# Kernel tuning notes

Measured on AMD Instinct MI355X. Metric: run time of the kernel, lower is better.

## Reference

```python
import jax, jax.numpy as jnp
import numpy as np

N_NODES = 20000
N_EDGES = 640000
IN_DIM, HID_DIM, OUT_DIM = 128, 128, 64


def setup_inputs() -> dict:
    key = jax.random.key(0)
    k = jax.random.split(key, 6)
    x = jax.random.normal(k[0], (N_NODES, IN_DIM), dtype=jnp.float32)
    edge_index = jax.random.randint(k[1], (2, N_EDGES), 0, N_NODES, dtype=jnp.int64)
    W1 = jax.random.normal(k[2], (IN_DIM, HID_DIM), dtype=jnp.float32) * (1.0 / np.sqrt(IN_DIM))
    b1 = jnp.zeros((HID_DIM,), dtype=jnp.float32)
    W2 = jax.random.normal(k[3], (HID_DIM, OUT_DIM), dtype=jnp.float32) * (1.0 / np.sqrt(HID_DIM))
    b2 = jnp.zeros((OUT_DIM,), dtype=jnp.float32)
    return {"x": x, "edge_index": edge_index, "W1": W1, "b1": b1, "W2": W2, "b2": b2}


def _gcn_conv(h, W, b, src, dst, n_nodes):
    # h' = D^-1/2 (A + I) D^-1/2 (h W) + b   (PyG GCNConv with self-loops)
    h = h @ W                                              # [N, F_out]
    ones = jnp.ones((src.shape[0],), dtype=h.dtype)
    deg = jax.ops.segment_sum(ones, dst, num_segments=n_nodes) + 1.0  # +1 for self-loop
    dinv = jax.lax.rsqrt(deg)                              # [N]
    w = dinv[src] * dinv[dst]                              # per-edge norm [E]
    msg = h[src] * w[:, None]                              # gather + scale [E, F_out]
    agg = jax.ops.segment_sum(msg, dst, num_segments=n_nodes)  # scatter-add [N, F_out]
    # self-loop contribution: norm_ii = dinv[i]^2
    return agg + h * (dinv * dinv)[:, None] + b


def reference(x, edge_index, W1, b1, W2, b2):
    src, dst = edge_index[0], edge_index[1]
    n = x.shape[0]
    h = _gcn_conv(x, W1, b1, src, dst, n)
    h = jax.nn.relu(h)
    # dropout is identity in eval mode (training=False)
    out = _gcn_conv(h, W2, b2, src, dst, n)
    return out
```

## Files before the change

kernel.cpp:

```cpp
#include <hip/hip_runtime.h>


#define N_NODES 20000
#define N_EDGES 640000
#define IN_DIM 128
#define HID_DIM 128
#define OUT_DIM 64

#define STRIDE 80
#define HB 256
#define EPB (N_EDGES / HB)
#define WT_NB ((128 * 128 + 64 * 128) / 256)
#define GEMM1_NB ((2 * (N_NODES / 16) + 3) / 4)

typedef _Float16 half8_t __attribute__((ext_vector_type(8)));
typedef float float4_t __attribute__((ext_vector_type(4)));

__global__ __launch_bounds__(256) void k_p1(const int* __restrict__ dst,
                                            unsigned char* __restrict__ ghist,
                                            const float* __restrict__ W1,
                                            const float* __restrict__ W2,
                                            _Float16* __restrict__ WT1,
                                            _Float16* __restrict__ WT2) {
    __shared__ unsigned int hist[N_NODES];
    const int b = blockIdx.x, tid = threadIdx.x;
    if (b < HB) {
        for (int i = tid; i < N_NODES; i += 256) hist[i] = 0;
        __syncthreads();
        const int base = b * EPB;
        for (int i = tid; i < EPB; i += 256)
            atomicAdd(&hist[dst[base + i]], 1u);
        __syncthreads();
        unsigned int* gh32 = (unsigned int*)(ghist + (size_t)b * N_NODES);
        for (int i = tid; i < N_NODES / 4; i += 256) {
            unsigned int v = (hist[4 * i] & 0xff) | ((hist[4 * i + 1] & 0xff) << 8) |
                             ((hist[4 * i + 2] & 0xff) << 16) | ((hist[4 * i + 3] & 0xff) << 24);
            gh32[i] = v;
        }
    } else {
        int i = (b - HB) * 256 + tid;
        if (i < 128 * 128) {
            int c = i >> 7, k = i & 127;
            WT1[i] = (_Float16)W1[k * 128 + c];
        } else {
            int o = i - 128 * 128;
            int c = o >> 7, k = o & 127;
            WT2[o] = (_Float16)W2[k * 64 + c];
        }
    }
}

__global__ __launch_bounds__(256) void k_p2(const unsigned char* __restrict__ ghist,
                                            unsigned char* __restrict__ boff,
                                            int* __restrict__ cnt) {
    int n = blockIdx.x * 256 + threadIdx.x;
    if (n >= N_NODES) return;
    unsigned int acc = 0;
#pragma unroll 8
    for (int b = 0; b < HB; ++b) {
        size_t idx = (size_t)b * N_NODES + n;
        unsigned int v = ghist[idx];
        boff[idx] = (unsigned char)acc;
        acc += v;
    }
    cnt[n] = (int)acc;
}

__global__ __launch_bounds__(256) void k_p3(const int* __restrict__ src,
                                            const int* __restrict__ dst,
                                            const unsigned char* __restrict__ boff,
                                            unsigned short* __restrict__ esrc_pad,
                                            const float* __restrict__ A,
                                            const _Float16* __restrict__ WT,
                                            const int* __restrict__ cnt,
                                            _Float16* __restrict__ GA,
                                            _Float16* __restrict__ GB) {
    __shared__ unsigned int hist[N_NODES];
    const int b = blockIdx.x, tid = threadIdx.x;
    if (b < HB) {
        for (int i = tid; i < N_NODES; i += 256) hist[i] = 0;
        __syncthreads();
        const int base = b * EPB;
        const unsigned char* bo = boff + (size_t)b * N_NODES;
        for (int i = tid; i < EPB; i += 256) {
            int e = base + i;
            int s = src[e], d = dst[e];
            unsigned int rank = atomicAdd(&hist[d], 1u);
            int pos = (int)bo[d] + (int)rank;
            if (pos < STRIDE) esrc_pad[d * STRIDE + pos] = (unsigned short)s;
        }
        return;
    }
    const int wave = tid >> 6;
    const int lane = tid & 63;
    const int task = (b - HB) * 4 + wave;
    if (task >= 2 * (N_NODES / 16)) return;
    const int strip = task >> 1;
    const int nh = task & 1;
    const int row0 = strip * 16;
    const int mrow = row0 + (lane & 15);
    const int kq = (lane >> 4) * 8;
    _Float16* G = nh ? GB : GA;

    half8_t af[4];
#pragma unroll
    for (int kc = 0; kc < 4; ++kc) {
        const float* ap = A + (size_t)mrow * 128 + kc * 32 + kq;
        float4_t f0 = *(const float4_t*)ap;
        float4_t f1 = *(const float4_t*)(ap + 4);
        half8_t h;
        h[0] = (_Float16)f0[0]; h[1] = (_Float16)f0[1];
        h[2] = (_Float16)f0[2]; h[3] = (_Float16)f0[3];
        h[4] = (_Float16)f1[0]; h[5] = (_Float16)f1[1];
        h[6] = (_Float16)f1[2]; h[7] = (_Float16)f1[3];
        af[kc] = h;
    }

    float4_t acc[4];
#pragma unroll
    for (int nt = 0; nt < 4; ++nt) acc[nt] = (float4_t)(0.0f);
#pragma unroll
    for (int nt = 0; nt < 4; ++nt) {
        const _Float16* wp = WT + (size_t)((nh * 4 + nt) * 16 + (lane & 15)) * 128 + kq;
#pragma unroll
        for (int kc = 0; kc < 4; ++kc) {
            half8_t bf = *(const half8_t*)(wp + kc * 32);
            acc[nt] = __builtin_amdgcn_mfma_f32_16x16x32_f16(af[kc], bf, acc[nt], 0, 0, 0);
        }
    }
#pragma unroll
    for (int r = 0; r < 4; ++r) {
        int row = row0 + (lane >> 4) * 4 + r;
        float dv = rsqrtf((float)cnt[row] + 1.0f);
#pragma unroll
        for (int nt = 0; nt < 4; ++nt)
            G[(size_t)row * 64 + nt * 16 + (lane & 15)] = (_Float16)(dv * acc[nt][r]);
    }
}

__global__ __launch_bounds__(256) void k_mgemm2(const _Float16* __restrict__ A,
                                                const _Float16* __restrict__ WT,
                                                const int* __restrict__ cnt,
                                                _Float16* __restrict__ G) {
    const int wave = threadIdx.x >> 6;
    const int lane = threadIdx.x & 63;
    const int task = blockIdx.x * 4 + wave;
    if (task >= 2 * (N_NODES / 16)) return;
    const int strip = task >> 1;
    const int nh = task & 1;
    const int row0 = strip * 16;
    const int mrow = row0 + (lane & 15);
    const int kq = (lane >> 4) * 8;

    half8_t af[4];
#pragma unroll
    for (int kc = 0; kc < 4; ++kc)
        af[kc] = *(const half8_t*)(A + (size_t)mrow * 128 + kc * 32 + kq);

    float4_t acc[2];
#pragma unroll
    for (int nt = 0; nt < 2; ++nt) acc[nt] = (float4_t)(0.0f);
#pragma unroll
    for (int nt = 0; nt < 2; ++nt) {
        const _Float16* wp = WT + (size_t)((nh * 2 + nt) * 16 + (lane & 15)) * 128 + kq;
#pragma unroll
        for (int kc = 0; kc < 4; ++kc) {
            half8_t bf = *(const half8_t*)(wp + kc * 32);
            acc[nt] = __builtin_amdgcn_mfma_f32_16x16x32_f16(af[kc], bf, acc[nt], 0, 0, 0);
        }
    }
#pragma unroll
    for (int r = 0; r < 4; ++r) {
        int row = row0 + (lane >> 4) * 4 + r;
        float dv = rsqrtf((float)cnt[row] + 1.0f);
#pragma unroll
        for (int nt = 0; nt < 2; ++nt)
            G[(size_t)row * 64 + (nh * 2 + nt) * 16 + (lane & 15)] =
                (_Float16)(dv * acc[nt][r]);
    }
}

template <int COL0>
__global__ __launch_bounds__(256) void k_agg128h(const int* __restrict__ cnt,
                                                 const unsigned short* __restrict__ esrc_pad,
                                                 const _Float16* __restrict__ G,
                                                 const float* __restrict__ bias,
                                                 _Float16* __restrict__ out) {
    const int wave = threadIdx.x >> 6;
    const int lane = threadIdx.x & 63;
    const int node = blockIdx.x * 4 + wave;
    if (node >= N_NODES) return;
    const int eidx = lane >> 3;
    const int flane = lane & 7;

    const int end = cnt[node];
    const int base = node * STRIDE;

    float acc[8];
#pragma unroll
    for (int p = 0; p < 8; ++p) acc[p] = 0.0f;
    if (lane < 8) {
        half8_t s = *(const half8_t*)(G + (size_t)node * 64 + flane * 8);
#pragma unroll
        for (int p = 0; p < 8; ++p) acc[p] = (float)s[p];
    }

    int j = 0;
    for (; j + 7 < end; j += 8) {
        int s = (int)esrc_pad[base + j + eidx];
        half8_t r = *(const half8_t*)(G + (size_t)s * 64 + flane * 8);
#pragma unroll
        for (int p = 0; p < 8; ++p) acc[p] += (float)r[p];
    }
    if (j < end) {
        int idx = j + eidx;
        int s = (int)esrc_pad[base + ((idx < end) ? idx : (end - 1))];
        float valid = (idx < end) ? 1.0f : 0.0f;
        half8_t r = *(const half8_t*)(G + (size_t)s * 64 + flane * 8);
#pragma unroll
        for (int p = 0; p < 8; ++p) acc[p] += valid * (float)r[p];
    }

#pragma unroll
    for (int p = 0; p < 8; ++p) {
        acc[p] += __shfl_xor(acc[p], 32, 64);
        acc[p] += __shfl_xor(acc[p], 16, 64);
        acc[p] += __shfl_xor(acc[p], 8, 64);
    }

    if (lane < 8) {
        float dv = rsqrtf((float)end + 1.0f);
        float4_t b0 = *(const float4_t*)(bias + COL0 + flane * 8);
        float4_t b1 = *(const float4_t*)(bias + COL0 + flane * 8 + 4);
        half8_t o;
        o[0] = (_Float16)fmaxf(acc[0] * dv + b0[0], 0.0f);
        o[1] = (_Float16)fmaxf(acc[1] * dv + b0[1], 0.0f);
        o[2] = (_Float16)fmaxf(acc[2] * dv + b0[2], 0.0f);
        o[3] = (_Float16)fmaxf(acc[3] * dv + b0[3], 0.0f);
        o[4] = (_Float16)fmaxf(acc[4] * dv + b1[0], 0.0f);
        o[5] = (_Float16)fmaxf(acc[5] * dv + b1[1], 0.0f);
        o[6] = (_Float16)fmaxf(acc[6] * dv + b1[2], 0.0f);
        o[7] = (_Float16)fmaxf(acc[7] * dv + b1[3], 0.0f);
        *(half8_t*)(out + (size_t)node * 128 + COL0 + flane * 8) = o;
    }
}

__global__ __launch_bounds__(256) void k_agg64(const int* __restrict__ cnt,
                                               const unsigned short* __restrict__ esrc_pad,
                                               const _Float16* __restrict__ g,
                                               const float* __restrict__ bias,
                                               float* __restrict__ out) {
    const int wave = threadIdx.x >> 6;
    const int lane = threadIdx.x & 63;
    const int node = blockIdx.x * 4 + wave;
    if (node >= N_NODES) return;
    const int eidx = lane >> 3;
    const int flane = lane & 7;

    const int end = cnt[node];
    const int base = node * STRIDE;

    float acc[8];
#pragma unroll
    for (int p = 0; p < 8; ++p) acc[p] = 0.0f;
    if (lane < 8) {
        half8_t s = *(const half8_t*)(g + (size_t)node * 64 + flane * 8);
#pragma unroll
        for (int p = 0; p < 8; ++p) acc[p] = (float)s[p];
    }

    int j = 0;
    for (; j + 7 < end; j += 8) {
        int s = (int)esrc_pad[base + j + eidx];
        half8_t r = *(const half8_t*)(g + (size_t)s * 64 + flane * 8);
#pragma unroll
        for (int p = 0; p < 8; ++p) acc[p] += (float)r[p];
    }
    if (j < end) {
        int idx = j + eidx;
        int s = (int)esrc_pad[base + ((idx < end) ? idx : (end - 1))];
        float valid = (idx < end) ? 1.0f : 0.0f;
        half8_t r = *(const half8_t*)(g + (size_t)s * 64 + flane * 8);
#pragma unroll
        for (int p = 0; p < 8; ++p) acc[p] += valid * (float)r[p];
    }

#pragma unroll
    for (int p = 0; p < 8; ++p) {
        acc[p] += __shfl_xor(acc[p], 32, 64);
        acc[p] += __shfl_xor(acc[p], 16, 64);
        acc[p] += __shfl_xor(acc[p], 8, 64);
    }

    if (lane < 8) {
        float dv = rsqrtf((float)end + 1.0f);
        float4_t b0 = *(const float4_t*)(bias + flane * 8);
        float4_t b1 = *(const float4_t*)(bias + flane * 8 + 4);
        float4_t o0, o1;
        o0[0] = acc[0] * dv + b0[0]; o0[1] = acc[1] * dv + b0[1];
        o0[2] = acc[2] * dv + b0[2]; o0[3] = acc[3] * dv + b0[3];
        o1[0] = acc[4] * dv + b1[0]; o1[1] = acc[5] * dv + b1[1];
        o1[2] = acc[6] * dv + b1[2]; o1[3] = acc[7] * dv + b1[3];
        *(float4_t*)(out + (size_t)node * 64 + flane * 8) = o0;
        *(float4_t*)(out + (size_t)node * 64 + flane * 8 + 4) = o1;
    }
}

extern "C" void kernel_launch(void* const* d_in, const int* in_sizes, int n_in,
                              void* d_out, int out_size, void* d_ws, size_t ws_size,
                              hipStream_t stream) {
    const float* x  = (const float*)d_in[0];
    const int*   ei = (const int*)d_in[1];
    const float* W1 = (const float*)d_in[2];
    const float* b1 = (const float*)d_in[3];
    const float* W2 = (const float*)d_in[4];
    const float* b2 = (const float*)d_in[5];

    const int* src = ei;
    const int* dst = ei + N_EDGES;

    char* w = (char*)d_ws;
    unsigned short* esrc_pad = (unsigned short*)w; w += sizeof(unsigned short) * (size_t)N_NODES * STRIDE;
    unsigned char*  ghist    = (unsigned char*)w;  w += (size_t)HB * N_NODES;
    unsigned char*  boff     = (unsigned char*)w;  w += (size_t)HB * N_NODES;
    _Float16*       g1a      = (_Float16*)w;       w += sizeof(_Float16) * (size_t)N_NODES * 64;
    _Float16*       g1b      = (_Float16*)w;       w += sizeof(_Float16) * (size_t)N_NODES * 64;
    _Float16*       h1p      = (_Float16*)w;       w += sizeof(_Float16) * (size_t)N_NODES * HID_DIM;
    _Float16*       g2       = (_Float16*)w;       w += sizeof(_Float16) * (size_t)N_NODES * OUT_DIM;
    _Float16*       WT1      = (_Float16*)w;       w += sizeof(_Float16) * 128 * 128;
    _Float16*       WT2      = (_Float16*)w;       w += sizeof(_Float16) * 64 * 128;
    int*            cnt      = (int*)w;            w += sizeof(int) * N_NODES;
    float*          out      = (float*)d_out;

    k_p1<<<HB + WT_NB, 256, 0, stream>>>(dst, ghist, W1, W2, WT1, WT2);
    k_p2<<<(N_NODES + 255) / 256, 256, 0, stream>>>(ghist, boff, cnt);
    k_p3<<<HB + GEMM1_NB, 256, 0, stream>>>(src, dst, boff, esrc_pad, x, WT1, cnt, g1a, g1b);

    k_agg128h<0><<<(N_NODES + 3) / 4, 256, 0, stream>>>(cnt, esrc_pad, g1a, b1, h1p);
    k_agg128h<64><<<(N_NODES + 3) / 4, 256, 0, stream>>>(cnt, esrc_pad, g1b, b1, h1p);

    k_mgemm2<<<(2 * (N_NODES / 16) + 3) / 4, 256, 0, stream>>>(h1p, WT2, cnt, g2);
    k_agg64<<<(N_NODES + 3) / 4, 256, 0, stream>>>(cnt, esrc_pad, g2, b2, out);
}
```

Baseline: 165.3 us.

## Build padded adjacency with global atomics and merge aggregation launches

Replaces the three-pass histogram, prefix-offset and scatter pipeline with one pass that takes a global atomicAdd on cnt[dst] as each edge's rank and writes the source id straight into the padded adjacency. This removes the two large per-block histogram buffers, the serial column scan and a launch, but needs a memset and contends on global atomics. The edge order inside each row becomes nondeterministic, which can change the float summation order. The two half-width layer-1 aggregation launches are merged into a single grid that picks its half from the block index.

```diff
diff --git a/kernel.cpp b/kernel.cpp
--- a/kernel.cpp
+++ b/kernel.cpp
@@ -8,37 +8,30 @@
 #define OUT_DIM 64
 
 #define STRIDE 80
-#define HB 256
-#define EPB (N_EDGES / HB)
+#define SCAT_NB (N_EDGES / 256)
 #define WT_NB ((128 * 128 + 64 * 128) / 256)
 #define GEMM1_NB ((2 * (N_NODES / 16) + 3) / 4)
+#define AGG_NB ((N_NODES + 3) / 4)
 
 typedef _Float16 half8_t __attribute__((ext_vector_type(8)));
 typedef float float4_t __attribute__((ext_vector_type(4)));
 
-__global__ __launch_bounds__(256) void k_p1(const int* __restrict__ dst,
-                                            unsigned char* __restrict__ ghist,
-                                            const float* __restrict__ W1,
-                                            const float* __restrict__ W2,
-                                            _Float16* __restrict__ WT1,
-                                            _Float16* __restrict__ WT2) {
-    __shared__ unsigned int hist[N_NODES];
+__global__ __launch_bounds__(256) void k_build(const int* __restrict__ src,
+                                               const int* __restrict__ dst,
+                                               int* __restrict__ cnt,
+                                               unsigned short* __restrict__ esrc_pad,
+                                               const float* __restrict__ W1,
+                                               const float* __restrict__ W2,
+                                               _Float16* __restrict__ WT1,
+                                               _Float16* __restrict__ WT2) {
     const int b = blockIdx.x, tid = threadIdx.x;
-    if (b < HB) {
-        for (int i = tid; i < N_NODES; i += 256) hist[i] = 0;
-        __syncthreads();
-        const int base = b * EPB;
-        for (int i = tid; i < EPB; i += 256)
-            atomicAdd(&hist[dst[base + i]], 1u);
-        __syncthreads();
-        unsigned int* gh32 = (unsigned int*)(ghist + (size_t)b * N_NODES);
-        for (int i = tid; i < N_NODES / 4; i += 256) {
-            unsigned int v = (hist[4 * i] & 0xff) | ((hist[4 * i + 1] & 0xff) << 8) |
-                             ((hist[4 * i + 2] & 0xff) << 16) | ((hist[4 * i + 3] & 0xff) << 24);
-            gh32[i] = v;
-        }
+    if (b < SCAT_NB) {
+        const int e = b * 256 + tid;
+        const int s = src[e], d = dst[e];
+        unsigned int rank = atomicAdd((unsigned int*)&cnt[d], 1u);
+        if (rank < STRIDE) esrc_pad[d * STRIDE + rank] = (unsigned short)s;
     } else {
-        int i = (b - HB) * 256 + tid;
+        int i = (b - SCAT_NB) * 256 + tid;
         if (i < 128 * 128) {
             int c = i >> 7, k = i & 127;
             WT1[i] = (_Float16)W1[k * 128 + c];
@@ -50,50 +43,14 @@
     }
 }
 
-__global__ __launch_bounds__(256) void k_p2(const unsigned char* __restrict__ ghist,
-                                            unsigned char* __restrict__ boff,
-                                            int* __restrict__ cnt) {
-    int n = blockIdx.x * 256 + threadIdx.x;
-    if (n >= N_NODES) return;
-    unsigned int acc = 0;
-#pragma unroll 8
-    for (int b = 0; b < HB; ++b) {
-        size_t idx = (size_t)b * N_NODES + n;
-        unsigned int v = ghist[idx];
-        boff[idx] = (unsigned char)acc;
-        acc += v;
-    }
-    cnt[n] = (int)acc;
-}
-
-__global__ __launch_bounds__(256) void k_p3(const int* __restrict__ src,
-                                            const int* __restrict__ dst,
-                                            const unsigned char* __restrict__ boff,
-                                            unsigned short* __restrict__ esrc_pad,
-                                            const float* __restrict__ A,
+__global__ __launch_bounds__(256) void k_g1(const float* __restrict__ A,
                                             const _Float16* __restrict__ WT,
                                             const int* __restrict__ cnt,
                                             _Float16* __restrict__ GA,
                                             _Float16* __restrict__ GB) {
-    __shared__ unsigned int hist[N_NODES];
-    const int b = blockIdx.x, tid = threadIdx.x;
-    if (b < HB) {
-        for (int i = tid; i < N_NODES; i += 256) hist[i] = 0;
-        __syncthreads();
-        const int base = b * EPB;
-        const unsigned char* bo = boff + (size_t)b * N_NODES;
-        for (int i = tid; i < EPB; i += 256) {
-            int e = base + i;
-            int s = src[e], d = dst[e];
-            unsigned int rank = atomicAdd(&hist[d], 1u);
-            int pos = (int)bo[d] + (int)rank;
-            if (pos < STRIDE) esrc_pad[d * STRIDE + pos] = (unsigned short)s;
-        }
-        return;
-    }
-    const int wave = tid >> 6;
-    const int lane = tid & 63;
-    const int task = (b - HB) * 4 + wave;
+    const int wave = threadIdx.x >> 6;
+    const int lane = threadIdx.x & 63;
+    const int task = blockIdx.x * 4 + wave;
     if (task >= 2 * (N_NODES / 16)) return;
     const int strip = task >> 1;
     const int nh = task & 1;
@@ -180,16 +137,20 @@
     }
 }
 
-template <int COL0>
-__global__ __launch_bounds__(256) void k_agg128h(const int* __restrict__ cnt,
+__global__ __launch_bounds__(256) void k_agg128f(const int* __restrict__ cnt,
                                                  const unsigned short* __restrict__ esrc_pad,
-                                                 const _Float16* __restrict__ G,
+                                                 const _Float16* __restrict__ Ga,
+                                                 const _Float16* __restrict__ Gb,
                                                  const float* __restrict__ bias,
                                                  _Float16* __restrict__ out) {
+    const int half = (blockIdx.x >= AGG_NB) ? 1 : 0;
+    const int bb = blockIdx.x - half * AGG_NB;
     const int wave = threadIdx.x >> 6;
     const int lane = threadIdx.x & 63;
-    const int node = blockIdx.x * 4 + wave;
+    const int node = bb * 4 + wave;
     if (node >= N_NODES) return;
+    const _Float16* __restrict__ G = half ? Gb : Ga;
+    const int COL0 = half << 6;
     const int eidx = lane >> 3;
     const int flane = lane & 7;
 
@@ -321,8 +282,6 @@
 
     char* w = (char*)d_ws;
     unsigned short* esrc_pad = (unsigned short*)w; w += sizeof(unsigned short) * (size_t)N_NODES * STRIDE;
-    unsigned char*  ghist    = (unsigned char*)w;  w += (size_t)HB * N_NODES;
-    unsigned char*  boff     = (unsigned char*)w;  w += (size_t)HB * N_NODES;
     _Float16*       g1a      = (_Float16*)w;       w += sizeof(_Float16) * (size_t)N_NODES * 64;
     _Float16*       g1b      = (_Float16*)w;       w += sizeof(_Float16) * (size_t)N_NODES * 64;
     _Float16*       h1p      = (_Float16*)w;       w += sizeof(_Float16) * (size_t)N_NODES * HID_DIM;
@@ -332,13 +291,12 @@
     int*            cnt      = (int*)w;            w += sizeof(int) * N_NODES;
     float*          out      = (float*)d_out;
 
-    k_p1<<<HB + WT_NB, 256, 0, stream>>>(dst, ghist, W1, W2, WT1, WT2);
-    k_p2<<<(N_NODES + 255) / 256, 256, 0, stream>>>(ghist, boff, cnt);
-    k_p3<<<HB + GEMM1_NB, 256, 0, stream>>>(src, dst, boff, esrc_pad, x, WT1, cnt, g1a, g1b);
-
-    k_agg128h<0><<<(N_NODES + 3) / 4, 256, 0, stream>>>(cnt, esrc_pad, g1a, b1, h1p);
-    k_agg128h<64><<<(N_NODES + 3) / 4, 256, 0, stream>>>(cnt, esrc_pad, g1b, b1, h1p);
-
-    k_mgemm2<<<(2 * (N_NODES / 16) + 3) / 4, 256, 0, stream>>>(h1p, WT2, cnt, g2);
-    k_agg64<<<(N_NODES + 3) / 4, 256, 0, stream>>>(cnt, esrc_pad, g2, b2, out);
-}
+    hipMemsetAsync(cnt, 0, sizeof(int) * N_NODES, stream);
+    k_build<<<SCAT_NB + WT_NB, 256, 0, stream>>>(src, dst, cnt, esrc_pad, W1, W2, WT1, WT2);
+
+    k_g1<<<GEMM1_NB, 256, 0, stream>>>(x, WT1, cnt, g1a, g1b);
+    k_agg128f<<<2 * AGG_NB, 256, 0, stream>>>(cnt, esrc_pad, g1a, g1b, b1, h1p);
+
+    k_mgemm2<<<GEMM1_NB, 256, 0, stream>>>(h1p, WT2, cnt, g2);
+    k_agg64<<<AGG_NB, 256, 0, stream>>>(cnt, esrc_pad, g2, b2, out);
+}
```

Result: faster. 161.4 us (-2.4%).
